# Kernel optimization log

Measured on AMD Instinct MI355X. Metric: run time of the kernel, lower is better.

Reference implementation:

```python
import jax, jax.numpy as jnp
import numpy as np

EMBED_DIM = 768
N_HEADS = 12
MLP_HID = 3072  # mlp_ratio 4.0
LN_EPS = 1e-6


def setup_inputs() -> dict:
    key = jax.random.key(0)
    ks = jax.random.split(key, 12)
    B, N, C = 4, 2048, EMBED_DIM
    s = 0.02
    return {
        "x": jax.random.normal(ks[0], (B, N, C), jnp.float32),
        "mask": jnp.ones((B, N), jnp.int32),
        "ln1_g": jnp.ones((C,), jnp.float32),
        "ln1_b": jnp.zeros((C,), jnp.float32),
        "qkv_w": jax.random.normal(ks[1], (C, 3 * C), jnp.float32) * s,
        "qkv_b": jnp.zeros((3 * C,), jnp.float32),
        "proj_w": jax.random.normal(ks[2], (C, C), jnp.float32) * s,
        "proj_b": jnp.zeros((C,), jnp.float32),
        "ln2_g": jnp.ones((C,), jnp.float32),
        "ln2_b": jnp.zeros((C,), jnp.float32),
        "fc1_w": jax.random.normal(ks[3], (C, MLP_HID), jnp.float32) * s,
        "fc1_b": jnp.zeros((MLP_HID,), jnp.float32),
        "fc2_w": jax.random.normal(ks[4], (MLP_HID, C), jnp.float32) * s,
        "fc2_b": jnp.zeros((C,), jnp.float32),
    }


def _layernorm(x, g, b):
    mu = jnp.mean(x, axis=-1, keepdims=True)
    var = jnp.mean(jnp.square(x - mu), axis=-1, keepdims=True)
    return (x - mu) * jax.lax.rsqrt(var + LN_EPS) * g + b


def _block(x, mask, ln1_g, ln1_b, qkv_w, qkv_b, proj_w, proj_b,
           ln2_g, ln2_b, fc1_w, fc1_b, fc2_w, fc2_b):
    B, N, C = x.shape
    H, D = N_HEADS, C // N_HEADS
    scale = D ** -0.5

    # --- attention (pre-norm) ---
    h = _layernorm(x, ln1_g, ln1_b)
    qkv = h @ qkv_w + qkv_b                      # [B,N,3C]
    qkv = qkv.reshape(B, N, 3, H, D).transpose(2, 0, 3, 1, 4)
    q, k, v = qkv[0], qkv[1], qkv[2]             # [B,H,N,D]
    scores = jnp.einsum("bhqd,bhkd->bhqk", q, k * scale)
    # 2-D mask path: (bsz, seq) -> (bsz, 1, seq, 1), mask queries
    m = mask[:, None, :, None]
    scores = jnp.where(m == 0, jnp.finfo(scores.dtype).min, scores)
    attn = jax.nn.softmax(scores, axis=-1)
    vals = jnp.einsum("bhqk,bhkd->bhqd", attn, v)
    vals = vals.transpose(0, 2, 1, 3).reshape(B, N, C)
    x = x + (vals @ proj_w + proj_b)

    # --- MLP (pre-norm, GELU exact) ---
    h = _layernorm(x, ln2_g, ln2_b)
    h = jax.nn.gelu(h @ fc1_w + fc1_b, approximate=False)
    x = x + (h @ fc2_w + fc2_b)
    return x


def reference(x, mask, ln1_g, ln1_b, qkv_w, qkv_b, proj_w, proj_b,
              ln2_g, ln2_b, fc1_w, fc1_b, fc2_w, fc2_b):
    return _block(x, mask, ln1_g, ln1_b, qkv_w, qkv_b, proj_w, proj_b,
                  ln2_g, ln2_b, fc1_w, fc1_b, fc2_w, fc2_b)
```

## Files before the change

### kernel.cpp

```cpp
#include <hip/hip_runtime.h>
#include <hip/hip_bf16.h>
#include <math.h>

using bf16 = __hip_bfloat16;
typedef short s16x8 __attribute__((ext_vector_type(8)));
typedef float f32x4 __attribute__((ext_vector_type(4)));
typedef float f32x16 __attribute__((ext_vector_type(16)));

#define LOG2E 1.4426950408889634f

__device__ inline unsigned short f2bf(float f) {
    bf16 h = __float2bfloat16(f);
    return __builtin_bit_cast(unsigned short, h);
}

__device__ inline float max3f(float a, float b, float c) {
    return fmaxf(fmaxf(a, b), c);
}

__device__ inline void gload_lds16(const void* g, void* l) {
    __builtin_amdgcn_global_load_lds(
        (const __attribute__((address_space(1))) void*)g,
        (__attribute__((address_space(3))) void*)l, 16, 0, 0);
}

__device__ inline float swap_halves(float x, int hi) {
    unsigned a = __builtin_bit_cast(unsigned, x);
    unsigned b = a;
    asm volatile("v_permlane32_swap_b32 %0, %1" : "+v"(a), "+v"(b));
    return hi ? __builtin_bit_cast(float, a) : __builtin_bit_cast(float, b);
}

__device__ inline unsigned cvtpk(float lo, float hi) {
    unsigned r;
    asm("v_cvt_pk_bf16_f32 %0, %1, %2" : "=v"(r) : "v"(lo), "v"(hi));
    return r;
}

__device__ inline s16x8 build_pfrag(float p0, float p1, float p2, float p3,
                                    float p4, float p5, float p6, float p7) {
    unsigned w01 = cvtpk(p0, p1);
    unsigned w23 = cvtpk(p2, p3);
    unsigned w45 = cvtpk(p4, p5);
    unsigned w67 = cvtpk(p6, p7);
    asm volatile("v_permlane32_swap_b32 %0, %1" : "+v"(w01), "+v"(w45));
    asm volatile("v_permlane32_swap_b32 %0, %1" : "+v"(w23), "+v"(w67));
    int4 t = {(int)w01, (int)w23, (int)w45, (int)w67};
    return __builtin_bit_cast(s16x8, t);
}

__global__ __launch_bounds__(256) void transpose_bf16(
    const float* __restrict__ in, bf16* __restrict__ out, int K, int N)
{
    __shared__ float tile[32][33];
    const int bx = blockIdx.x * 32;
    const int by = blockIdx.y * 32;
    const int tx = threadIdx.x, ty = threadIdx.y;
    #pragma unroll
    for (int i = 0; i < 32; i += 8)
        tile[ty + i][tx] = in[(size_t)(by + ty + i) * N + bx + tx];
    __syncthreads();
    #pragma unroll
    for (int i = 0; i < 32; i += 8)
        out[(size_t)(bx + ty + i) * K + by + tx] = __float2bfloat16(tile[tx][ty + i]);
}

__global__ __launch_bounds__(256) void ln_kernel(
    const float* __restrict__ x, const float* __restrict__ g,
    const float* __restrict__ bb, bf16* __restrict__ out)
{
    const int row = blockIdx.x;
    const float* xr = x + (size_t)row * 768;
    float v[3];
    float s = 0.f, s2 = 0.f;
    #pragma unroll
    for (int i = 0; i < 3; ++i) {
        v[i] = xr[threadIdx.x + i * 256];
        s += v[i];
        s2 += v[i] * v[i];
    }
    #pragma unroll
    for (int off = 1; off < 64; off <<= 1) {
        s += __shfl_xor(s, off);
        s2 += __shfl_xor(s2, off);
    }
    __shared__ float rs[4], rs2[4];
    const int wave = threadIdx.x >> 6;
    if ((threadIdx.x & 63) == 0) { rs[wave] = s; rs2[wave] = s2; }
    __syncthreads();
    s = rs[0] + rs[1] + rs[2] + rs[3];
    s2 = rs2[0] + rs2[1] + rs2[2] + rs2[3];
    const float mu = s * (1.f / 768.f);
    const float var = s2 * (1.f / 768.f) - mu * mu;
    const float r = rsqrtf(var + 1e-6f);
    bf16* orow = out + (size_t)row * 768;
    #pragma unroll
    for (int i = 0; i < 3; ++i) {
        const int col = threadIdx.x + i * 256;
        orow[col] = __float2bfloat16((v[i] - mu) * r * g[col] + bb[col]);
    }
}

#define BM 128
#define BN 128
#define BK 64

template <int EPI>
__global__ __launch_bounds__(256) void gemm_bt(
    const bf16* __restrict__ A, const bf16* __restrict__ Bt,
    const float* __restrict__ bias, const float* __restrict__ resid,
    void* __restrict__ outp, const int* __restrict__ mask,
    bf16* __restrict__ Qb, bf16* __restrict__ Kb, bf16* __restrict__ Vt,
    int M, int N, int K)
{
    __shared__ alignas(16) char smem[32768];
    char* As = smem;
    char* Bs = smem + 16384;
    const int tid = threadIdx.x;
    const int lane = tid & 63;
    const int wave = tid >> 6;
    const int wm = wave >> 1, wn = wave & 1;
    const int lr = lane & 15, lg = lane >> 4;
    const int bm = blockIdx.x, bn = blockIdx.y;

    f32x4 acc[4][4] = {};

    const size_t a_row0 = (size_t)bm * BM;
    const size_t b_row0 = (size_t)bn * BN;

    for (int kt = 0; kt < K; kt += BK) {
        #pragma unroll
        for (int i = 0; i < 4; ++i) {
            const int id = tid + i * 256;
            const int row = id >> 3, c = id & 7;
            const int cs = (c ^ (row & 7)) * 8;
            gload_lds16(A + (a_row0 + row) * K + kt + cs, As + id * 16);
            gload_lds16(Bt + (b_row0 + row) * K + kt + cs, Bs + id * 16);
        }
        __syncthreads();
        #pragma unroll
        for (int ks = 0; ks < 2; ++ks) {
            s16x8 af[4], bfr[4];
            #pragma unroll
            for (int mf = 0; mf < 4; ++mf) {
                const int row = wm * 64 + mf * 16 + lr;
                const int c = ks * 4 + lg;
                af[mf] = *reinterpret_cast<const s16x8*>(As + row * 128 + ((c ^ (row & 7)) * 16));
            }
            #pragma unroll
            for (int nf = 0; nf < 4; ++nf) {
                const int row = wn * 64 + nf * 16 + lr;
                const int c = ks * 4 + lg;
                bfr[nf] = *reinterpret_cast<const s16x8*>(Bs + row * 128 + ((c ^ (row & 7)) * 16));
            }
            #pragma unroll
            for (int mf = 0; mf < 4; ++mf)
                #pragma unroll
                for (int nf = 0; nf < 4; ++nf)
                    acc[mf][nf] = __builtin_amdgcn_mfma_f32_16x16x32_bf16(
                        af[mf], bfr[nf], acc[mf][nf], 0, 0, 0);
        }
        __syncthreads();
    }

    if (EPI == 3) {
        const int rq = bn / 6;
        const int bb_ = bm >> 4;
        if (rq == 2) {
            char* Ws = smem + wave * 8192;
            #pragma unroll
            for (int nf = 0; nf < 4; ++nf) {
                const int cl = nf * 16 + lr;
                const int gn = bn * 128 + wn * 64 + nf * 16 + lr;
                const float bs = bias[gn];
                #pragma unroll
                for (int mf = 0; mf < 4; ++mf) {
                    unsigned short pk[4];
                    #pragma unroll
                    for (int i = 0; i < 4; ++i) pk[i] = f2bf(acc[mf][nf][i] + bs);
                    const int slot = (2 * mf + (lg >> 1)) ^ (cl & 7);
                    *reinterpret_cast<long long*>(Ws + cl * 128 + slot * 16 + (lg & 1) * 8) =
                        *reinterpret_cast<const long long*>(pk);
                }
            }
            __syncthreads();
            const int nb = (bm * 128 + wm * 64) & 2047;
            const int cb = (bn - 12) * 128 + wn * 64;
            #pragma unroll
            for (int r = 0; r < 8; ++r) {
                const int cl = r * 8 + (lane >> 3);
                const int j = lane & 7;
                const int4 vv = *reinterpret_cast<const int4*>(
                    Ws + cl * 128 + ((j ^ (cl & 7)) * 16));
                const int c = cb + cl;
                const int hh = c >> 6, dd = c & 63;
                *reinterpret_cast<int4*>(
                    Vt + ((size_t)(bb_ * 12 + hh) * 64 + dd) * 2048 + nb + j * 8) = vv;
            }
        } else {
            const int cb = bn * 128 - rq * 768 + wn * 64;
            bf16* dst = (rq == 0) ? Qb : Kb;
            #pragma unroll
            for (int mf = 0; mf < 4; ++mf) {
                #pragma unroll
                for (int i = 0; i < 4; ++i) {
                    const int gm = bm * 128 + wm * 64 + mf * 16 + 4 * lg + i;
                    const int n = gm & 2047;
                    const float msc = (rq == 0) ? (mask[gm] ? 0.125f : 0.f) : 1.f;
                    #pragma unroll
                    for (int nf = 0; nf < 4; ++nf) {
                        const int c = cb + nf * 16 + lr;
                        const int h = c >> 6, d = c & 63;
                        const int gn = bn * 128 + wn * 64 + nf * 16 + lr;
                        const float v = (acc[mf][nf][i] + bias[gn]) * msc;
                        dst[((size_t)(bb_ * 12 + h) * 2048 + n) * 64 + d] =
                            __float2bfloat16(v);
                    }
                }
            }
        }
        return;
    }

    #pragma unroll
    for (int mf = 0; mf < 4; ++mf) {
        #pragma unroll
        for (int i = 0; i < 4; ++i) {
            const int gm = bm * BM + wm * 64 + mf * 16 + 4 * lg + i;
            #pragma unroll
            for (int nf = 0; nf < 4; ++nf) {
                const int gn = bn * BN + wn * 64 + nf * 16 + lr;
                float v = acc[mf][nf][i] + bias[gn];
                if (EPI == 1) v += resid[(size_t)gm * N + gn];
                if (EPI == 2) {
                    const float x3 = v * v * v;
                    const float z = fmaf(x3, 0.044715f, v) * 2.3022080f;
                    const float e = __builtin_amdgcn_exp2f(z);
                    v = v - v * __builtin_amdgcn_rcpf(1.f + e);
                }
                if (EPI == 1)
                    reinterpret_cast<float*>(outp)[(size_t)gm * N + gn] = v;
                else
                    reinterpret_cast<bf16*>(outp)[(size_t)gm * N + gn] = __float2bfloat16(v);
            }
        }
    }
}

__global__ __launch_bounds__(256, 3) void attn_kernel(
    const bf16* __restrict__ Qb, const bf16* __restrict__ Kb,
    const bf16* __restrict__ Vt, bf16* __restrict__ out)
{
    __shared__ alignas(16) char Ks[2][64 * 128];
    __shared__ alignas(16) char Vs[2][64 * 128];

    const int lin = blockIdx.x;
    const int xcd = lin & 7, slot = lin >> 3;
    const int pair = xcd * 6 + (slot >> 4);
    const int qb = slot & 15;
    const int b = pair / 12, h = pair % 12;

    const int tid = threadIdx.x, lane = tid & 63, wave = tid >> 6;
    const int lq = lane & 31;
    const int hi = lane >> 5;
    const size_t bh = (size_t)(b * 12 + h);
    const bf16* Kh = Kb + bh * 2048 * 64;
    const bf16* Vh = Vt + bh * 64 * 2048;
    const int q0w = qb * 128 + wave * 32;

    s16x8 qf[4];
    {
        const bf16* qp = Qb + (bh * 2048 + q0w + lq) * 64 + 8 * hi;
        #pragma unroll
        for (int ks = 0; ks < 4; ++ks)
            qf[ks] = *reinterpret_cast<const s16x8*>(qp + 16 * ks);
    }

    int sKoff0, sKoff1, dst0, dst1;
    size_t sVoff0, sVoff1;
    {
        const int id0 = tid;
        const int R0 = id0 >> 4;
        const int u0 = (id0 & 15) ^ (R0 & 15);
        const int rt0 = 2 * R0 + (u0 >> 3), s80 = (u0 & 7) * 8;
        sKoff0 = rt0 * 64 + s80;
        sVoff0 = (size_t)rt0 * 2048 + s80;
        dst0 = id0 * 16;
        const int id1 = tid + 256;
        const int R1 = id1 >> 4;
        const int u1 = (id1 & 15) ^ (R1 & 15);
        const int rt1 = 2 * R1 + (u1 >> 3), s81 = (u1 & 7) * 8;
        sKoff1 = rt1 * 64 + s81;
        sVoff1 = (size_t)rt1 * 2048 + s81;
        dst1 = id1 * 16;
    }

    const int rh = lq >> 1;
    const int m7 = rh & 7;
    const int rbase = rh * 256 + (((((lq & 1) << 3) ^ (rh & 8))) << 4);

    float m_r = -1e30f, l_r = 0.f;
    f32x16 o0 = {}, o1 = {};

    #define STAGE(buf, kb)                                                    \
        do {                                                                  \
            gload_lds16(Kh + (kb) * 4096 + sKoff0, Ks[buf] + dst0);           \
            gload_lds16(Vh + (kb) * 64 + sVoff0, Vs[buf] + dst0);             \
            gload_lds16(Kh + (kb) * 4096 + sKoff1, Ks[buf] + dst1);           \
            gload_lds16(Vh + (kb) * 64 + sVoff1, Vs[buf] + dst1);             \
        } while (0)

    STAGE(0, 0);
    __syncthreads();
    int cur = 0;

    for (int kb = 0; kb < 32; ++kb) {
        if (kb < 31) STAGE(cur ^ 1, kb + 1);
        const char* Kc = Ks[cur] + rbase;
        const char* Vc = Vs[cur] + rbase;

        f32x16 st0 = {}, st1 = {};
        __builtin_amdgcn_s_setprio(1);
        #pragma unroll
        for (int ks = 0; ks < 4; ++ks) {
            const int so = (((2 * ks + hi) ^ m7) << 4);
            const s16x8 kf0 = *reinterpret_cast<const s16x8*>(Kc + so);
            st0 = __builtin_amdgcn_mfma_f32_32x32x16_bf16(kf0, qf[ks], st0, 0, 0, 0);
            const s16x8 kf1 = *reinterpret_cast<const s16x8*>(Kc + 4096 + so);
            st1 = __builtin_amdgcn_mfma_f32_32x32x16_bf16(kf1, qf[ks], st1, 0, 0, 0);
        }
        __builtin_amdgcn_s_setprio(0);

        float a0 = max3f(st0[0], st0[1], st0[2]);
        float a1 = max3f(st0[3], st0[4], st0[5]);
        float a2 = max3f(st0[6], st0[7], st0[8]);
        float a3 = max3f(st0[9], st0[10], st0[11]);
        float a4 = max3f(st0[12], st0[13], st0[14]);
        float b0 = max3f(st1[0], st1[1], st1[2]);
        float b1 = max3f(st1[3], st1[4], st1[5]);
        float b2 = max3f(st1[6], st1[7], st1[8]);
        float b3 = max3f(st1[9], st1[10], st1[11]);
        float b4 = max3f(st1[12], st1[13], st1[14]);
        a0 = max3f(a0, a1, a2);
        a3 = max3f(a3, a4, st0[15]);
        b0 = max3f(b0, b1, b2);
        b3 = max3f(b3, b4, st1[15]);
        float mx = fmaxf(fmaxf(a0, a3), fmaxf(b0, b3));
        mx = fmaxf(mx, swap_halves(mx, hi));
        const float ml = mx * LOG2E;
        if (!__all(ml - m_r <= 8.0f)) {
            const float mnew = fmaxf(m_r, ml);
            const float alpha = __builtin_amdgcn_exp2f(m_r - mnew);
            m_r = mnew;
            l_r *= alpha;
            #pragma unroll
            for (int r = 0; r < 16; ++r) { o0[r] *= alpha; o1[r] *= alpha; }
        }
        float p0[16], p1[16];
        float rsa = 0.f, rsb = 0.f;
        #pragma unroll
        for (int r = 0; r < 16; ++r) {
            p0[r] = __builtin_amdgcn_exp2f(fmaf(st0[r], LOG2E, -m_r));
            p1[r] = __builtin_amdgcn_exp2f(fmaf(st1[r], LOG2E, -m_r));
            rsa += p0[r];
            rsb += p1[r];
        }
        float rs = rsa + rsb;
        rs += swap_halves(rs, hi);
        l_r += rs;

        const s16x8 pf00 = build_pfrag(p0[0], p0[1], p0[2], p0[3], p0[4], p0[5], p0[6], p0[7]);
        const s16x8 pf01 = build_pfrag(p0[8], p0[9], p0[10], p0[11], p0[12], p0[13], p0[14], p0[15]);
        const s16x8 pf10 = build_pfrag(p1[0], p1[1], p1[2], p1[3], p1[4], p1[5], p1[6], p1[7]);
        const s16x8 pf11 = build_pfrag(p1[8], p1[9], p1[10], p1[11], p1[12], p1[13], p1[14], p1[15]);

        __builtin_amdgcn_s_setprio(1);
        #pragma unroll
        for (int kf4 = 0; kf4 < 4; ++kf4) {
            const s16x8 pf = (kf4 == 0) ? pf00 : (kf4 == 1) ? pf01
                           : (kf4 == 2) ? pf10 : pf11;
            const int so = (((2 * kf4 + hi) ^ m7) << 4);
            const s16x8 vf0 = *reinterpret_cast<const s16x8*>(Vc + so);
            o0 = __builtin_amdgcn_mfma_f32_32x32x16_bf16(vf0, pf, o0, 0, 0, 0);
            const s16x8 vf1 = *reinterpret_cast<const s16x8*>(Vc + 4096 + so);
            o1 = __builtin_amdgcn_mfma_f32_32x32x16_bf16(vf1, pf, o1, 0, 0, 0);
        }
        __builtin_amdgcn_s_setprio(0);

        __syncthreads();
        cur ^= 1;
    }
    #undef STAGE

    const float rl = 1.0f / l_r;
    bf16* orow = out + (size_t)(b * 2048 + q0w + lq) * 768 + h * 64;
    #pragma unroll
    for (int g = 0; g < 4; ++g) {
        unsigned short pk0[4], pk1[4];
        #pragma unroll
        for (int i = 0; i < 4; ++i) {
            pk0[i] = f2bf(o0[4 * g + i] * rl);
            pk1[i] = f2bf(o1[4 * g + i] * rl);
        }
        const int d0 = 8 * g + 4 * hi;
        *reinterpret_cast<int2*>(orow + d0) = *reinterpret_cast<const int2*>(pk0);
        *reinterpret_cast<int2*>(orow + 32 + d0) = *reinterpret_cast<const int2*>(pk1);
    }
}

extern "C" void kernel_launch(void* const* d_in, const int* in_sizes, int n_in,
                              void* d_out, int out_size, void* d_ws, size_t ws_size,
                              hipStream_t stream)
{
    (void)in_sizes; (void)n_in; (void)out_size; (void)ws_size;
    const float* x      = (const float*)d_in[0];
    const int*   mask   = (const int*)d_in[1];
    const float* ln1_g  = (const float*)d_in[2];
    const float* ln1_b  = (const float*)d_in[3];
    const float* qkv_w  = (const float*)d_in[4];
    const float* qkv_b  = (const float*)d_in[5];
    const float* proj_w = (const float*)d_in[6];
    const float* proj_b = (const float*)d_in[7];
    const float* ln2_g  = (const float*)d_in[8];
    const float* ln2_b  = (const float*)d_in[9];
    const float* fc1_w  = (const float*)d_in[10];
    const float* fc1_b  = (const float*)d_in[11];
    const float* fc2_w  = (const float*)d_in[12];
    const float* fc2_b  = (const float*)d_in[13];
    float* out = (float*)d_out;
    char* ws = (char*)d_ws;

    bf16*  Wt_qkv  = (bf16*)(ws + 0);
    bf16*  Wt_proj = (bf16*)(ws + 3538944);
    bf16*  Wt_fc1  = (bf16*)(ws + 4718592);
    bf16*  Wt_fc2  = (bf16*)(ws + 9437184);
    bf16*  hbuf    = (bf16*)(ws + 14155776);
    bf16*  attnout = (bf16*)(ws + 64487424);
    float* x1      = (float*)(ws + 77070336);
    bf16*  h2      = (bf16*)(ws + 102236160);
    bf16*  a1      = (bf16*)(ws + 114819072);
    bf16*  Qb      = (bf16*)(ws + 114819072);
    bf16*  Kb      = (bf16*)(ws + 127401984);
    bf16*  Vt      = (bf16*)(ws + 139984896);

    const dim3 tb(32, 8);
    transpose_bf16<<<dim3(2304 / 32, 768 / 32), tb, 0, stream>>>(qkv_w, Wt_qkv, 768, 2304);
    transpose_bf16<<<dim3(768 / 32, 768 / 32), tb, 0, stream>>>(proj_w, Wt_proj, 768, 768);
    transpose_bf16<<<dim3(3072 / 32, 768 / 32), tb, 0, stream>>>(fc1_w, Wt_fc1, 768, 3072);
    transpose_bf16<<<dim3(768 / 32, 3072 / 32), tb, 0, stream>>>(fc2_w, Wt_fc2, 3072, 768);

    ln_kernel<<<8192, 256, 0, stream>>>(x, ln1_g, ln1_b, hbuf);
    gemm_bt<3><<<dim3(64, 18), 256, 0, stream>>>(hbuf, Wt_qkv, qkv_b, nullptr, nullptr,
                                                 mask, Qb, Kb, Vt, 8192, 2304, 768);
    attn_kernel<<<768, 256, 0, stream>>>(Qb, Kb, Vt, attnout);
    gemm_bt<1><<<dim3(64, 6), 256, 0, stream>>>(attnout, Wt_proj, proj_b, x, x1,
                                                nullptr, nullptr, nullptr, nullptr, 8192, 768, 768);
    ln_kernel<<<8192, 256, 0, stream>>>(x1, ln2_g, ln2_b, h2);
    gemm_bt<2><<<dim3(64, 24), 256, 0, stream>>>(h2, Wt_fc1, fc1_b, nullptr, a1,
                                                 nullptr, nullptr, nullptr, nullptr, 8192, 3072, 768);
    gemm_bt<1><<<dim3(64, 6), 256, 0, stream>>>(a1, Wt_fc2, fc2_b, x1, out,
                                                nullptr, nullptr, nullptr, nullptr, 8192, 768, 3072);
}
```

Before: 282.7 us.

## Replace GEMM with 8-wave 256x128 double-buffered pipelined kernel

```diff
diff --git a/kernel.cpp b/kernel.cpp
--- a/kernel.cpp
+++ b/kernel.cpp
@@ -101,73 +101,128 @@
     }
 }
 
-#define BM 128
-#define BN 128
-#define BK 64
-
 template <int EPI>
-__global__ __launch_bounds__(256) void gemm_bt(
+__global__ __launch_bounds__(512, 2) void gemm8(
     const bf16* __restrict__ A, const bf16* __restrict__ Bt,
     const float* __restrict__ bias, const float* __restrict__ resid,
     void* __restrict__ outp, const int* __restrict__ mask,
     bf16* __restrict__ Qb, bf16* __restrict__ Kb, bf16* __restrict__ Vt,
     int M, int N, int K)
 {
-    __shared__ alignas(16) char smem[32768];
-    char* As = smem;
-    char* Bs = smem + 16384;
+    __shared__ alignas(16) char smem[98304];
     const int tid = threadIdx.x;
     const int lane = tid & 63;
     const int wave = tid >> 6;
     const int wm = wave >> 1, wn = wave & 1;
     const int lr = lane & 15, lg = lane >> 4;
     const int bm = blockIdx.x, bn = blockIdx.y;
+    const size_t a_row0 = (size_t)bm * 256;
+    const size_t b_row0 = (size_t)bn * 128;
+
+    const int dA0 = tid, dA1 = tid + 512;
+    const int rA0 = dA0 >> 2, cA0 = (dA0 & 3) ^ (rA0 & 3);
+    const int rA1 = dA1 >> 2, cA1 = (dA1 & 3) ^ (rA1 & 3);
+    const int rB  = tid >> 2,  cB  = (tid & 3) ^ (rB & 3);
+    const bf16* srcA0 = A + (a_row0 + rA0) * K + cA0 * 8;
+    const bf16* srcA1 = A + (a_row0 + rA1) * K + cA1 * 8;
+    const bf16* srcB  = Bt + (b_row0 + rB) * K + cB * 8;
+
+    int aoff[4], boff[4];
+    #pragma unroll
+    for (int mf = 0; mf < 4; ++mf)
+        aoff[mf] = (wm * 64 + mf * 16 + lr) * 64 + ((lg ^ (lr & 3)) << 4);
+    #pragma unroll
+    for (int nf = 0; nf < 4; ++nf)
+        boff[nf] = 65536 + (wn * 64 + nf * 16 + lr) * 64 + ((lg ^ (lr & 3)) << 4);
 
     f32x4 acc[4][4] = {};
-
-    const size_t a_row0 = (size_t)bm * BM;
-    const size_t b_row0 = (size_t)bn * BN;
-
-    for (int kt = 0; kt < K; kt += BK) {
-        #pragma unroll
-        for (int i = 0; i < 4; ++i) {
-            const int id = tid + i * 256;
-            const int row = id >> 3, c = id & 7;
-            const int cs = (c ^ (row & 7)) * 8;
-            gload_lds16(A + (a_row0 + row) * K + kt + cs, As + id * 16);
-            gload_lds16(Bt + (b_row0 + row) * K + kt + cs, Bs + id * 16);
-        }
-        __syncthreads();
-        #pragma unroll
-        for (int ks = 0; ks < 2; ++ks) {
-            s16x8 af[4], bfr[4];
-            #pragma unroll
-            for (int mf = 0; mf < 4; ++mf) {
-                const int row = wm * 64 + mf * 16 + lr;
-                const int c = ks * 4 + lg;
-                af[mf] = *reinterpret_cast<const s16x8*>(As + row * 128 + ((c ^ (row & 7)) * 16));
-            }
-            #pragma unroll
-            for (int nf = 0; nf < 4; ++nf) {
-                const int row = wn * 64 + nf * 16 + lr;
-                const int c = ks * 4 + lg;
-                bfr[nf] = *reinterpret_cast<const s16x8*>(Bs + row * 128 + ((c ^ (row & 7)) * 16));
-            }
-            #pragma unroll
-            for (int mf = 0; mf < 4; ++mf)
-                #pragma unroll
-                for (int nf = 0; nf < 4; ++nf)
-                    acc[mf][nf] = __builtin_amdgcn_mfma_f32_16x16x32_bf16(
-                        af[mf], bfr[nf], acc[mf][nf], 0, 0, 0);
-        }
-        __syncthreads();
-    }
+    const int NT = K >> 6;
+
+#define STAGE_HALF(p_, h_, kt_)                                                        \
+    do {                                                                               \
+        gload_lds16(srcA0 + (kt_) + (h_) * 32,                                         \
+                    smem + (p_) * 32768 + (h_) * 16384 + dA0 * 16);                    \
+        gload_lds16(srcA1 + (kt_) + (h_) * 32,                                         \
+                    smem + (p_) * 32768 + (h_) * 16384 + dA1 * 16);                    \
+        gload_lds16(srcB + (kt_) + (h_) * 32,                                          \
+                    smem + 65536 + (p_) * 16384 + (h_) * 8192 + tid * 16);             \
+    } while (0)
+
+#define MFMA8(n0, n1)                                                                  \
+    do {                                                                               \
+        __builtin_amdgcn_s_setprio(1);                                                 \
+        _Pragma("unroll")                                                              \
+        for (int mf = 0; mf < 4; ++mf) {                                               \
+            acc[mf][n0] = __builtin_amdgcn_mfma_f32_16x16x32_bf16(af[mf], bA, acc[mf][n0], 0, 0, 0); \
+            acc[mf][n1] = __builtin_amdgcn_mfma_f32_16x16x32_bf16(af[mf], bB, acc[mf][n1], 0, 0, 0); \
+        }                                                                              \
+        __builtin_amdgcn_s_setprio(0);                                                 \
+    } while (0)
+
+    STAGE_HALF(0, 0, 0);
+    STAGE_HALF(0, 1, 0);
+    asm volatile("s_waitcnt vmcnt(3)" ::: "memory");
+    __builtin_amdgcn_s_barrier();
+
+    int p = 0;
+    for (int t = 0; t < NT; ++t, p ^= 1) {
+        const int pa = p * 32768;
+        const int pb = p * 16384;
+        const bool pre = (t + 1 < NT);
+        const int ktn = (t + 1) * 64;
+        s16x8 af[4], bA, bB;
+
+        #pragma unroll
+        for (int mf = 0; mf < 4; ++mf)
+            af[mf] = *reinterpret_cast<const s16x8*>(smem + pa + aoff[mf]);
+        bA = *reinterpret_cast<const s16x8*>(smem + pb + boff[0]);
+        bB = *reinterpret_cast<const s16x8*>(smem + pb + boff[1]);
+        if (pre) STAGE_HALF(p ^ 1, 0, ktn);
+        __builtin_amdgcn_s_barrier();
+        asm volatile("s_waitcnt lgkmcnt(0)" ::: "memory");
+        __builtin_amdgcn_sched_barrier(0);
+        MFMA8(0, 1);
+        __builtin_amdgcn_s_barrier();
+
+        bA = *reinterpret_cast<const s16x8*>(smem + pb + boff[2]);
+        bB = *reinterpret_cast<const s16x8*>(smem + pb + boff[3]);
+        if (pre) STAGE_HALF(p ^ 1, 1, ktn);
+        __builtin_amdgcn_s_barrier();
+        asm volatile("s_waitcnt lgkmcnt(0)" ::: "memory");
+        __builtin_amdgcn_sched_barrier(0);
+        MFMA8(2, 3);
+        if (pre) { asm volatile("s_waitcnt vmcnt(6)" ::: "memory"); }
+        else     { asm volatile("s_waitcnt vmcnt(0)" ::: "memory"); }
+        __builtin_amdgcn_s_barrier();
+
+        #pragma unroll
+        for (int mf = 0; mf < 4; ++mf)
+            af[mf] = *reinterpret_cast<const s16x8*>(smem + pa + 16384 + aoff[mf]);
+        bA = *reinterpret_cast<const s16x8*>(smem + pb + 8192 + boff[0]);
+        bB = *reinterpret_cast<const s16x8*>(smem + pb + 8192 + boff[1]);
+        __builtin_amdgcn_s_barrier();
+        asm volatile("s_waitcnt lgkmcnt(0)" ::: "memory");
+        __builtin_amdgcn_sched_barrier(0);
+        MFMA8(0, 1);
+        __builtin_amdgcn_s_barrier();
+
+        bA = *reinterpret_cast<const s16x8*>(smem + pb + 8192 + boff[2]);
+        bB = *reinterpret_cast<const s16x8*>(smem + pb + 8192 + boff[3]);
+        __builtin_amdgcn_s_barrier();
+        asm volatile("s_waitcnt lgkmcnt(0)" ::: "memory");
+        __builtin_amdgcn_sched_barrier(0);
+        MFMA8(2, 3);
+        asm volatile("s_waitcnt vmcnt(3)" ::: "memory");
+        __builtin_amdgcn_s_barrier();
+    }
+#undef STAGE_HALF
+#undef MFMA8
 
     if (EPI == 3) {
         const int rq = bn / 6;
-        const int bb_ = bm >> 4;
+        const int bb_ = bm >> 3;
         if (rq == 2) {
-            char* Ws = smem + wave * 8192;
+            const int wso = wave * 8192;
             #pragma unroll
             for (int nf = 0; nf < 4; ++nf) {
                 const int cl = nf * 16 + lr;
@@ -179,19 +234,19 @@
                     #pragma unroll
                     for (int i = 0; i < 4; ++i) pk[i] = f2bf(acc[mf][nf][i] + bs);
                     const int slot = (2 * mf + (lg >> 1)) ^ (cl & 7);
-                    *reinterpret_cast<long long*>(Ws + cl * 128 + slot * 16 + (lg & 1) * 8) =
+                    *reinterpret_cast<long long*>(smem + wso + cl * 128 + slot * 16 + (lg & 1) * 8) =
                         *reinterpret_cast<const long long*>(pk);
                 }
             }
             __syncthreads();
-            const int nb = (bm * 128 + wm * 64) & 2047;
+            const int nb = (bm * 256 + wm * 64) & 2047;
             const int cb = (bn - 12) * 128 + wn * 64;
             #pragma unroll
             for (int r = 0; r < 8; ++r) {
                 const int cl = r * 8 + (lane >> 3);
                 const int j = lane & 7;
                 const int4 vv = *reinterpret_cast<const int4*>(
-                    Ws + cl * 128 + ((j ^ (cl & 7)) * 16));
+                    smem + wso + cl * 128 + ((j ^ (cl & 7)) * 16));
                 const int c = cb + cl;
                 const int hh = c >> 6, dd = c & 63;
                 *reinterpret_cast<int4*>(
@@ -204,7 +259,7 @@
             for (int mf = 0; mf < 4; ++mf) {
                 #pragma unroll
                 for (int i = 0; i < 4; ++i) {
-                    const int gm = bm * 128 + wm * 64 + mf * 16 + 4 * lg + i;
+                    const int gm = bm * 256 + wm * 64 + mf * 16 + 4 * lg + i;
                     const int n = gm & 2047;
                     const float msc = (rq == 0) ? (mask[gm] ? 0.125f : 0.f) : 1.f;
                     #pragma unroll
@@ -226,10 +281,10 @@
     for (int mf = 0; mf < 4; ++mf) {
         #pragma unroll
         for (int i = 0; i < 4; ++i) {
-            const int gm = bm * BM + wm * 64 + mf * 16 + 4 * lg + i;
+            const int gm = bm * 256 + wm * 64 + mf * 16 + 4 * lg + i;
             #pragma unroll
             for (int nf = 0; nf < 4; ++nf) {
-                const int gn = bn * BN + wn * 64 + nf * 16 + lr;
+                const int gn = bn * 128 + wn * 64 + nf * 16 + lr;
                 float v = acc[mf][nf][i] + bias[gn];
                 if (EPI == 1) v += resid[(size_t)gm * N + gn];
                 if (EPI == 2) {
@@ -450,14 +505,14 @@
     transpose_bf16<<<dim3(768 / 32, 3072 / 32), tb, 0, stream>>>(fc2_w, Wt_fc2, 3072, 768);
 
     ln_kernel<<<8192, 256, 0, stream>>>(x, ln1_g, ln1_b, hbuf);
-    gemm_bt<3><<<dim3(64, 18), 256, 0, stream>>>(hbuf, Wt_qkv, qkv_b, nullptr, nullptr,
-                                                 mask, Qb, Kb, Vt, 8192, 2304, 768);
+    gemm8<3><<<dim3(32, 18), 512, 0, stream>>>(hbuf, Wt_qkv, qkv_b, nullptr, nullptr,
+                                               mask, Qb, Kb, Vt, 8192, 2304, 768);
     attn_kernel<<<768, 256, 0, stream>>>(Qb, Kb, Vt, attnout);
-    gemm_bt<1><<<dim3(64, 6), 256, 0, stream>>>(attnout, Wt_proj, proj_b, x, x1,
-                                                nullptr, nullptr, nullptr, nullptr, 8192, 768, 768);
+    gemm8<1><<<dim3(32, 6), 512, 0, stream>>>(attnout, Wt_proj, proj_b, x, x1,
+                                              nullptr, nullptr, nullptr, nullptr, 8192, 768, 768);
     ln_kernel<<<8192, 256, 0, stream>>>(x1, ln2_g, ln2_b, h2);
-    gemm_bt<2><<<dim3(64, 24), 256, 0, stream>>>(h2, Wt_fc1, fc1_b, nullptr, a1,
-                                                 nullptr, nullptr, nullptr, nullptr, 8192, 3072, 768);
-    gemm_bt<1><<<dim3(64, 6), 256, 0, stream>>>(a1, Wt_fc2, fc2_b, x1, out,
-                                                nullptr, nullptr, nullptr, nullptr, 8192, 768, 3072);
-}
+    gemm8<2><<<dim3(32, 24), 512, 0, stream>>>(h2, Wt_fc1, fc1_b, nullptr, a1,
+                                               nullptr, nullptr, nullptr, nullptr, 8192, 3072, 768);
+    gemm8<1><<<dim3(32, 6), 512, 0, stream>>>(a1, Wt_fc2, fc2_b, x1, out,
+                                              nullptr, nullptr, nullptr, nullptr, 8192, 768, 3072);
+}
```

Measured after the change: 307.4 us. 8.7% more time.
